# Kernel optimization log

Hardware: AMD Instinct MI355X
Metric: run time of the kernel (lower is better)

The kernel has to match this reference:

```python
import jax, jax.numpy as jnp
import numpy as np

B, C, H, W = 64, 256, 64, 64
E = 4                      # num_experts
CELL = 8
OUT = CELL * CELL + 1      # 65
EPS_BN = 1e-5
EPS_LB = 1e-6


def setup_inputs() -> dict:
    key = jax.random.key(0)
    ks = jax.random.split(key, 6)
    x = jax.random.normal(ks[0], (B, C, H, W), dtype=jnp.float32)
    w_experts = jax.random.normal(ks[1], (E, C, OUT), dtype=jnp.float32) * 0.05
    b_experts = jax.random.normal(ks[2], (E, OUT), dtype=jnp.float32) * 0.05
    w_gate = jax.random.normal(ks[3], (C, E), dtype=jnp.float32) * 0.05
    b_gate = jax.random.normal(ks[4], (E,), dtype=jnp.float32) * 0.05
    gamma = jnp.ones((OUT,), dtype=jnp.float32)
    beta = jnp.zeros((OUT,), dtype=jnp.float32)
    return {"x": x, "w_experts": w_experts, "b_experts": b_experts,
            "w_gate": w_gate, "b_gate": b_gate, "gamma": gamma, "beta": beta}


def pixel_shuffle(t, r):
    n, ch, h, w = t.shape
    nc = ch // (r * r)
    t = t.reshape(n, nc, r, r, h, w)
    t = t.transpose(0, 1, 4, 2, 5, 3)
    return t.reshape(n, nc, h * r, w * r)


def reference(x, w_experts, b_experts, w_gate, b_gate, gamma, beta):
    x = jax.nn.relu(x)
    xh = x.transpose(0, 2, 3, 1)                       # [B,H,W,C]

    # gating: global-avg-pool -> linear -> softmax -> hard top-1
    pooled = xh.mean(axis=(1, 2))                      # [B,C]
    gate = jax.nn.softmax(pooled @ w_gate + b_gate, axis=-1)
    idx = jnp.argmax(gate, axis=-1)                    # [B]

    # load-balancing KL(usage || uniform)
    usage = jnp.mean(jax.nn.one_hot(idx, E, dtype=xh.dtype), axis=0) + EPS_LB
    usage = usage / usage.sum()
    lb_loss = jnp.sum(usage * (jnp.log(usage) - jnp.log(jnp.full_like(usage, 1.0 / E))))

    # fused gather->grouped-GEMM (per-sample expert weight selection)
    w_sel = w_experts[idx]                             # [B,C,OUT]
    b_sel = b_experts[idx]                             # [B,OUT]
    y = jnp.einsum('bhwc,bco->bhwo', xh, w_sel) + b_sel[:, None, None, :]
    y = y.transpose(0, 3, 1, 2)                        # [B,OUT,H,W]

    # BatchNorm2d (training mode: batch statistics, biased variance)
    mean = y.mean(axis=(0, 2, 3), keepdims=True)
    var = y.var(axis=(0, 2, 3), keepdims=True)
    logits = (y - mean) / jnp.sqrt(var + EPS_BN)
    logits = logits * gamma[None, :, None, None] + beta[None, :, None, None]

    prob = jax.nn.softmax(logits, axis=1)[:, :-1]      # drop dustbin channel
    prob = pixel_shuffle(prob, CELL)                   # [B,1,H*8,W*8]
    prob = prob[:, 0]                                  # squeeze dim=1
    return logits, prob, lb_loss
```

## Files before the change

### kernel.cpp

```cpp
#include <hip/hip_runtime.h>
#include <stdint.h>
#include <math.h>

#define B_    64
#define C_    256
#define HW_   4096
#define E_    4
#define OUT_  65
#define NPAD_ 80

#define LOGITS_SZ (B_*OUT_*HW_)
#define PROB_SZ   (B_*512*512)

#define POOLED_OFF 0u
#define IDX_OFF    65536u
#define BNSUM_OFF  65792u
#define BNSS_OFF   66112u
#define WT_OFF     67072u
#define YB_OFF     230912u
#define CLEAR_BYTES 66432u

typedef float  f4 __attribute__((ext_vector_type(4)));
typedef short  s8 __attribute__((ext_vector_type(8)));

__device__ __forceinline__ uint32_t f2bf(float f){
  uint32_t u = __float_as_uint(f);
  return (u + 0x7FFFu + ((u >> 16) & 1u)) >> 16;
}
__device__ __forceinline__ uint32_t pk(float lo, float hi){
  return f2bf(lo) | (f2bf(hi) << 16);
}
__device__ __forceinline__ float bf2f(uint32_t u){
  return __uint_as_float((u & 0xFFFFu) << 16);
}


__global__ __launch_bounds__(256) void k_prep(const float* __restrict__ x,
                                              uint16_t* __restrict__ xb,
                                              float* __restrict__ pooled){
  __shared__ float pool_lds[64];
  int bid = blockIdx.x;
  int b = bid >> 7, ct = (bid >> 5) & 3, pt = bid & 31;
  int t = threadIdx.x;
  int cg = t & 7, pgg = t >> 3;
  int c0 = ct*64 + cg*8;
  int p0 = pt*128 + pgg*4;
  if (t < 64) pool_lds[t] = 0.f;
  __syncthreads();

  float v[8][4]; float s[8];
  const float* xp = x + ((size_t)(b*C_ + c0))*HW_ + p0;
#pragma unroll
  for (int r = 0; r < 8; ++r){
    float4 f = *(const float4*)(xp + (size_t)r*HW_);
    v[r][0]=fmaxf(f.x,0.f); v[r][1]=fmaxf(f.y,0.f);
    v[r][2]=fmaxf(f.z,0.f); v[r][3]=fmaxf(f.w,0.f);
    s[r] = v[r][0]+v[r][1]+v[r][2]+v[r][3];
  }
  int ksg  = ct*2 + (cg >> 2);
  int quad = cg & 3;
#pragma unroll
  for (int pp = 0; pp < 4; ++pp){
    int p = p0 + pp;
    uint16_t* dst = xb + ((((size_t)(b*256 + (p>>4))*8 + ksg)*64)
                          + (size_t)((p&15)*4 + quad))*8;
    uint4 w;
    w.x = pk(v[0][pp], v[1][pp]); w.y = pk(v[2][pp], v[3][pp]);
    w.z = pk(v[4][pp], v[5][pp]); w.w = pk(v[6][pp], v[7][pp]);
    *(uint4*)dst = w;
  }
#pragma unroll
  for (int r = 0; r < 8; ++r){
    float vv = s[r];
    vv += __shfl_xor(vv, 8);
    vv += __shfl_xor(vv, 16);
    vv += __shfl_xor(vv, 32);
    if ((t & 56) == 0)
      atomicAdd(&pool_lds[cg*8 + r], vv);
  }
  __syncthreads();
  if (t < 64) atomicAdd(pooled + b*C_ + ct*64 + t, pool_lds[t]);
}

__global__ void k_wtgate(const float* __restrict__ w_experts,
                         const float* __restrict__ w_gate,
                         const float* __restrict__ b_gate,
                         const float* __restrict__ pooled_sum,
                         uint16_t* __restrict__ Wt,
                         int* __restrict__ idx_ws,
                         float* __restrict__ out_lb){
  int bid = blockIdx.x;
  int t = threadIdx.x;
  if (bid < 320){
    if (t >= 32) return;
    int e = bid / NPAD_, o = bid % NPAD_;
    int ks = t >> 2, quad = t & 3;
    int c = t*8;
    float a[8];
    if (o < OUT_){
      const float* src = w_experts + (size_t)e*C_*OUT_ + o;
#pragma unroll
      for (int j = 0; j < 8; ++j) a[j] = src[(size_t)(c+j)*OUT_];
    } else {
#pragma unroll
      for (int j = 0; j < 8; ++j) a[j] = 0.f;
    }
    uint4 w;
    w.x = pk(a[0],a[1]); w.y = pk(a[2],a[3]);
    w.z = pk(a[4],a[5]); w.w = pk(a[6],a[7]);
    uint16_t* dst = Wt + ((((size_t)(e*5 + (o>>4))*8 + ks)*64)
                          + (size_t)((o&15)*4 + quad))*8;
    *(uint4*)dst = w;
    return;
  }
  __shared__ float gl[64][4];
  __shared__ int ish[64];
  int b = t >> 2, e = t & 3;
  float dot = 0.f;
  const float* pr = pooled_sum + b*C_;
  for (int c = 0; c < C_; c += 4){
    float4 p4 = *(const float4*)(pr + c);
    dot += p4.x*w_gate[c*4+e] + p4.y*w_gate[(c+1)*4+e]
         + p4.z*w_gate[(c+2)*4+e] + p4.w*w_gate[(c+3)*4+e];
  }
  gl[b][e] = dot * (1.f/4096.f) + b_gate[e];
  __syncthreads();
  if (t < 64){
    float best = gl[t][0]; int bi = 0;
    for (int ee = 1; ee < 4; ++ee){ float vv = gl[t][ee]; if (vv > best){best = vv; bi = ee;} }
    idx_ws[t] = bi; ish[t] = bi;
  }
  __syncthreads();
  if (t == 0){
    int cnt[4] = {0,0,0,0};
    for (int bb = 0; bb < 64; ++bb) cnt[ish[bb]]++;
    double u[4], S = 0.0;
    for (int ee = 0; ee < 4; ++ee){ u[ee] = cnt[ee]/64.0 + 1e-6; S += u[ee]; }
    double lb = 0.0;
    for (int ee = 0; ee < 4; ++ee){ double uu = u[ee]/S; lb += uu*(log(uu) - log(0.25)); }
    *out_lb = (float)lb;
  }
}

__global__ __launch_bounds__(256) void k_gemm(const uint16_t* __restrict__ xb,
                                              const uint16_t* __restrict__ Wt,
                                              const int* __restrict__ idx_ws,
                                              const float* __restrict__ b_experts,
                                              uint16_t* __restrict__ yb,
                                              float* __restrict__ bnsum,
                                              float* __restrict__ bnss){
  __shared__ float2 bnp[NPAD_*4];
  int bid = blockIdx.x;
  int b = bid >> 4, pt = bid & 15;
  int t = threadIdx.x;
  int w = t >> 6, lane = t & 63;
  int l15 = lane & 15, quad = lane >> 4;
  int lid = l15*4 + quad;
  int e = idx_ws[b];
  int p0 = pt*256 + w*64;
  const uint16_t* ap = xb + ((size_t)(b*256 + pt*16 + w*4))*4096 + (size_t)lid*8;
  const uint16_t* bp = Wt + (size_t)e*5*4096 + (size_t)lid*8;

  f4 acc[4][5];
#pragma unroll
  for (int mt=0; mt<4; ++mt)
#pragma unroll
    for (int nt=0; nt<5; ++nt){ f4 z = {0.f,0.f,0.f,0.f}; acc[mt][nt] = z; }

#pragma unroll
  for (int ks = 0; ks < 8; ++ks){
    s8 av[4], bv[5];
#pragma unroll
    for (int mt=0; mt<4; ++mt) av[mt] = *(const s8*)(ap + (size_t)mt*4096 + ks*512);
#pragma unroll
    for (int nt=0; nt<5; ++nt) bv[nt] = *(const s8*)(bp + (size_t)nt*4096 + ks*512);
#pragma unroll
    for (int mt=0; mt<4; ++mt)
#pragma unroll
      for (int nt=0; nt<5; ++nt)
        acc[mt][nt] = __builtin_amdgcn_mfma_f32_16x16x32_bf16(av[mt], bv[nt], acc[mt][nt], 0, 0, 0);
  }

#pragma unroll
  for (int nt=0; nt<5; ++nt){
    int o = nt*16 + l15;
    float bias = (o < OUT_) ? b_experts[e*OUT_ + o] : 0.f;
    float s1 = 0.f, s2 = 0.f;
#pragma unroll
    for (int mt=0; mt<4; ++mt){
#pragma unroll
      for (int r=0; r<4; ++r){
        float vv = acc[mt][nt][r] + bias;
        acc[mt][nt][r] = vv;
        s1 += vv; s2 += vv*vv;
      }
      if (o < OUT_){
        size_t base = ((size_t)(b*OUT_ + o))*HW_ + p0 + mt*16 + quad*4;
        uint2 st;
        st.x = pk(acc[mt][nt][0], acc[mt][nt][1]);
        st.y = pk(acc[mt][nt][2], acc[mt][nt][3]);
        *(uint2*)(yb + base) = st;
      }
    }
    s1 += __shfl_xor(s1, 16); s1 += __shfl_xor(s1, 32);
    s2 += __shfl_xor(s2, 16); s2 += __shfl_xor(s2, 32);
    if (quad == 0) bnp[(nt*16 + l15)*4 + w] = make_float2(s1, s2);
  }
  __syncthreads();
  if (t < OUT_){
    float2 a0 = bnp[t*4+0], a1 = bnp[t*4+1], a2 = bnp[t*4+2], a3 = bnp[t*4+3];
    atomicAdd(bnsum + t, a0.x+a1.x+a2.x+a3.x);
    atomicAdd(bnss  + t, a0.y+a1.y+a2.y+a3.y);
  }
}

__global__ __launch_bounds__(256) void k_final(const uint16_t* __restrict__ yb,
                                               const float* __restrict__ bnsum,
                                               const float* __restrict__ bnss,
                                               const float* __restrict__ gamma,
                                               const float* __restrict__ beta,
                                               float* __restrict__ out_logits,
                                               float* __restrict__ out_prob){
  __shared__ float lt[OUT_*132];
  __shared__ float2 ss[OUT_];
  int bid = blockIdx.x;
  int b = bid >> 5, pt = bid & 31;
  int p0 = pt*128;
  int t = threadIdx.x;
  if (t < OUT_){
    const float invN = 1.f/(float)(B_*HW_);
    float mean = bnsum[t]*invN;
    float var  = bnss[t]*invN - mean*mean;
    float sc   = gamma[t] / sqrtf(var + 1e-5f);
    ss[t] = make_float2(sc, beta[t] - mean*sc);
  }
  __syncthreads();

  int prr = t & 15, og = t >> 4;
#pragma unroll
  for (int oi = 0; oi < 5; ++oi){
    int o = og + oi*16;
    if (o < OUT_){
      size_t base = ((size_t)(b*OUT_ + o))*HW_ + p0 + prr*8;
      uint4 raw = *(const uint4*)(yb + base);
      float f[8];
      f[0]=bf2f(raw.x); f[1]=bf2f(raw.x>>16);
      f[2]=bf2f(raw.y); f[3]=bf2f(raw.y>>16);
      f[4]=bf2f(raw.z); f[5]=bf2f(raw.z>>16);
      f[6]=bf2f(raw.w); f[7]=bf2f(raw.w>>16);
      float2 sv = ss[o];
#pragma unroll
      for (int k=0;k<8;++k) f[k] = f[k]*sv.x + sv.y;
      float4 w0 = make_float4(f[0],f[1],f[2],f[3]);
      float4 w1 = make_float4(f[4],f[5],f[6],f[7]);
      *(float4*)(out_logits + base)     = w0;
      *(float4*)(out_logits + base + 4) = w1;
      float* lp = lt + o*132 + prr*8;
      *(float4*)(lp)     = w0;
      *(float4*)(lp + 4) = w1;
    }
  }
  __syncthreads();

  if (t < 128){
    float m = -1e30f;
    for (int o = 0; o < OUT_; ++o) m = fmaxf(m, lt[o*132 + t]);
    float ssum = 0.f;
    for (int o = 0; o < OUT_; ++o) ssum += __expf(lt[o*132 + t] - m);
    float inv = 1.f/ssum;
    int P = p0 + t;
    int h = P >> 6, wd = P & 63;
    float* pb = out_prob + ((size_t)b << 18) + (size_t)(h*8)*512 + wd*8;
#pragma unroll
    for (int r1 = 0; r1 < 8; ++r1){
      float4 q0, q1;
      q0.x = __expf(lt[(r1*8+0)*132+t]-m)*inv;
      q0.y = __expf(lt[(r1*8+1)*132+t]-m)*inv;
      q0.z = __expf(lt[(r1*8+2)*132+t]-m)*inv;
      q0.w = __expf(lt[(r1*8+3)*132+t]-m)*inv;
      q1.x = __expf(lt[(r1*8+4)*132+t]-m)*inv;
      q1.y = __expf(lt[(r1*8+5)*132+t]-m)*inv;
      q1.z = __expf(lt[(r1*8+6)*132+t]-m)*inv;
      q1.w = __expf(lt[(r1*8+7)*132+t]-m)*inv;
      *(float4*)(pb + r1*512)     = q0;
      *(float4*)(pb + r1*512 + 4) = q1;
    }
  }
}

extern "C" void kernel_launch(void* const* d_in, const int* in_sizes, int n_in,
                              void* d_out, int out_size, void* d_ws, size_t ws_size,
                              hipStream_t stream){
  const float* x         = (const float*)d_in[0];
  const float* w_experts = (const float*)d_in[1];
  const float* b_experts = (const float*)d_in[2];
  const float* w_gate    = (const float*)d_in[3];
  const float* b_gate    = (const float*)d_in[4];
  const float* gamma     = (const float*)d_in[5];
  const float* beta      = (const float*)d_in[6];

  float* out = (float*)d_out;
  char*  ws  = (char*)d_ws;
  float*     pooled = (float*)(ws + POOLED_OFF);
  int*       idxw   = (int*)(ws + IDX_OFF);
  float*     bnsum  = (float*)(ws + BNSUM_OFF);
  float*     bnss   = (float*)(ws + BNSS_OFF);
  uint16_t*  Wt     = (uint16_t*)(ws + WT_OFF);
  uint16_t*  ybm    = (uint16_t*)(ws + YB_OFF);
  uint16_t*  xbm    = (uint16_t*)d_out;

  float* logits = out;
  float* prob   = out + LOGITS_SZ;
  float* lb     = out + LOGITS_SZ + PROB_SZ;

  hipMemsetAsync(ws, 0, CLEAR_BYTES, stream);
  k_prep  <<<8192, 256, 0, stream>>>(x, xbm, pooled);
  k_wtgate<<<321, 256, 0, stream>>>(w_experts, w_gate, b_gate, pooled, Wt, idxw, lb);
  k_gemm  <<<1024, 256, 0, stream>>>(xbm, Wt, idxw, b_experts, ybm, bnsum, bnss);
  k_final <<<2048, 256, 0, stream>>>(ybm, bnsum, bnss, gamma, beta, logits, prob);
}
```

Before: 499.2 us.

## Fuse GEMM and BatchNorm/softmax epilogue via cooperative grid sync

Merges the grouped GEMM and the BN-normalize/softmax/pixel-shuffle kernel into one cooperative kernel. Accumulators stay in registers across a grid-wide sync, so the bf16 intermediate y never round-trips through global memory. It also folds the expert-weight transpose into the prep kernel and spreads the BN-statistic atomics over 8 slots to reduce contention. In exchange it requires all 1024 blocks to be co-resident, and it stages logits through LDS in two halves. A two-kernel fallback runs if the cooperative launch fails.

```diff
diff --git a/kernel.cpp b/kernel.cpp
--- a/kernel.cpp
+++ b/kernel.cpp
@@ -1,6 +1,9 @@
 #include <hip/hip_runtime.h>
+#include <hip/hip_cooperative_groups.h>
 #include <stdint.h>
 #include <math.h>
+
+namespace cg = cooperative_groups;
 
 #define B_    64
 #define C_    256
@@ -14,11 +17,11 @@
 
 #define POOLED_OFF 0u
 #define IDX_OFF    65536u
-#define BNSUM_OFF  65792u
-#define BNSS_OFF   66112u
-#define WT_OFF     67072u
-#define YB_OFF     230912u
-#define CLEAR_BYTES 66432u
+#define BNS_OFF    65792u
+#define BNSS_OFF   68352u
+#define CLEAR_BYTES 70912u
+#define WT_OFF     70912u
+#define YB_OFF     234752u
 
 typedef float  f4 __attribute__((ext_vector_type(4)));
 typedef short  s8 __attribute__((ext_vector_type(8)));
@@ -36,14 +39,41 @@
 
 
 __global__ __launch_bounds__(256) void k_prep(const float* __restrict__ x,
+                                              const float* __restrict__ w_experts,
                                               uint16_t* __restrict__ xb,
+                                              uint16_t* __restrict__ Wt,
                                               float* __restrict__ pooled){
   __shared__ float pool_lds[64];
   int bid = blockIdx.x;
+  int t = threadIdx.x;
+
+  if (bid >= 8192){
+    if (t >= 32) return;
+    int pid = bid - 8192;
+    int e = pid / NPAD_, o = pid % NPAD_;
+    int ks = t >> 2, quad = t & 3;
+    int c = t*8;
+    float a[8];
+    if (o < OUT_){
+      const float* src = w_experts + (size_t)e*C_*OUT_ + o;
+#pragma unroll
+      for (int j = 0; j < 8; ++j) a[j] = src[(size_t)(c+j)*OUT_];
+    } else {
+#pragma unroll
+      for (int j = 0; j < 8; ++j) a[j] = 0.f;
+    }
+    uint4 wv;
+    wv.x = pk(a[0],a[1]); wv.y = pk(a[2],a[3]);
+    wv.z = pk(a[4],a[5]); wv.w = pk(a[6],a[7]);
+    uint16_t* dst = Wt + ((((size_t)(e*5 + (o>>4))*8 + ks)*64)
+                          + (size_t)((o&15)*4 + quad))*8;
+    *(uint4*)dst = wv;
+    return;
+  }
+
   int b = bid >> 7, ct = (bid >> 5) & 3, pt = bid & 31;
-  int t = threadIdx.x;
-  int cg = t & 7, pgg = t >> 3;
-  int c0 = ct*64 + cg*8;
+  int cg_ = t & 7, pgg = t >> 3;
+  int c0 = ct*64 + cg_*8;
   int p0 = pt*128 + pgg*4;
   if (t < 64) pool_lds[t] = 0.f;
   __syncthreads();
@@ -57,8 +87,8 @@
     v[r][2]=fmaxf(f.z,0.f); v[r][3]=fmaxf(f.w,0.f);
     s[r] = v[r][0]+v[r][1]+v[r][2]+v[r][3];
   }
-  int ksg  = ct*2 + (cg >> 2);
-  int quad = cg & 3;
+  int ksg  = ct*2 + (cg_ >> 2);
+  int quad = cg_ & 3;
 #pragma unroll
   for (int pp = 0; pp < 4; ++pp){
     int p = p0 + pp;
@@ -76,45 +106,20 @@
     vv += __shfl_xor(vv, 16);
     vv += __shfl_xor(vv, 32);
     if ((t & 56) == 0)
-      atomicAdd(&pool_lds[cg*8 + r], vv);
+      atomicAdd(&pool_lds[cg_*8 + r], vv);
   }
   __syncthreads();
   if (t < 64) atomicAdd(pooled + b*C_ + ct*64 + t, pool_lds[t]);
 }
 
-__global__ void k_wtgate(const float* __restrict__ w_experts,
-                         const float* __restrict__ w_gate,
-                         const float* __restrict__ b_gate,
-                         const float* __restrict__ pooled_sum,
-                         uint16_t* __restrict__ Wt,
-                         int* __restrict__ idx_ws,
-                         float* __restrict__ out_lb){
-  int bid = blockIdx.x;
-  int t = threadIdx.x;
-  if (bid < 320){
-    if (t >= 32) return;
-    int e = bid / NPAD_, o = bid % NPAD_;
-    int ks = t >> 2, quad = t & 3;
-    int c = t*8;
-    float a[8];
-    if (o < OUT_){
-      const float* src = w_experts + (size_t)e*C_*OUT_ + o;
-#pragma unroll
-      for (int j = 0; j < 8; ++j) a[j] = src[(size_t)(c+j)*OUT_];
-    } else {
-#pragma unroll
-      for (int j = 0; j < 8; ++j) a[j] = 0.f;
-    }
-    uint4 w;
-    w.x = pk(a[0],a[1]); w.y = pk(a[2],a[3]);
-    w.z = pk(a[4],a[5]); w.w = pk(a[6],a[7]);
-    uint16_t* dst = Wt + ((((size_t)(e*5 + (o>>4))*8 + ks)*64)
-                          + (size_t)((o&15)*4 + quad))*8;
-    *(uint4*)dst = w;
-    return;
-  }
+__global__ void k_lb(const float* __restrict__ pooled_sum,
+                     const float* __restrict__ w_gate,
+                     const float* __restrict__ b_gate,
+                     int* __restrict__ idx_ws,
+                     float* __restrict__ out_lb){
   __shared__ float gl[64][4];
   __shared__ int ish[64];
+  int t = threadIdx.x;
   int b = t >> 2, e = t & 3;
   float dot = 0.f;
   const float* pr = pooled_sum + b*C_;
@@ -142,13 +147,166 @@
   }
 }
 
-__global__ __launch_bounds__(256) void k_gemm(const uint16_t* __restrict__ xb,
-                                              const uint16_t* __restrict__ Wt,
-                                              const int* __restrict__ idx_ws,
-                                              const float* __restrict__ b_experts,
-                                              uint16_t* __restrict__ yb,
-                                              float* __restrict__ bnsum,
-                                              float* __restrict__ bnss){
+__global__ __launch_bounds__(256, 4) void k_fused(
+    const uint16_t* __restrict__ xb, const uint16_t* __restrict__ Wt,
+    const int* __restrict__ idx_ws, const float* __restrict__ b_experts,
+    const float* __restrict__ gamma, const float* __restrict__ beta,
+    float* __restrict__ bnsum, float* __restrict__ bnss,
+    float* __restrict__ out_logits, float* __restrict__ out_prob){
+  __shared__ union ShMem {
+    float2 bnp[NPAD_*4];
+    struct { uint16_t lt[OUT_*136]; float2 ss[OUT_]; } fin;
+  } sh;
+
+  int bid = blockIdx.x;
+  int b = bid >> 4, pt = bid & 15;
+  int t = threadIdx.x;
+  int w = t >> 6, lane = t & 63;
+  int l15 = lane & 15, quad = lane >> 4;
+  int lid = l15*4 + quad;
+  int e = idx_ws[b];
+
+  int p0 = pt*256 + w*64;
+  const uint16_t* ap = xb + ((size_t)(b*256 + pt*16 + w*4))*4096 + (size_t)lid*8;
+  const uint16_t* bp = Wt + (size_t)e*5*4096 + (size_t)lid*8;
+
+  f4 acc[4][5];
+#pragma unroll
+  for (int mt=0; mt<4; ++mt)
+#pragma unroll
+    for (int nt=0; nt<5; ++nt){ f4 z = {0.f,0.f,0.f,0.f}; acc[mt][nt] = z; }
+
+#pragma unroll
+  for (int ks = 0; ks < 8; ++ks){
+    s8 bv[5];
+#pragma unroll
+    for (int nt=0; nt<5; ++nt) bv[nt] = *(const s8*)(bp + (size_t)nt*4096 + ks*512);
+#pragma unroll
+    for (int mt=0; mt<4; ++mt){
+      s8 av = *(const s8*)(ap + (size_t)mt*4096 + ks*512);
+#pragma unroll
+      for (int nt=0; nt<5; ++nt)
+        acc[mt][nt] = __builtin_amdgcn_mfma_f32_16x16x32_bf16(av, bv[nt], acc[mt][nt], 0, 0, 0);
+    }
+  }
+
+#pragma unroll
+  for (int nt=0; nt<5; ++nt){
+    int o = nt*16 + l15;
+    float bias = (o < OUT_) ? b_experts[e*OUT_ + o] : 0.f;
+    float s1 = 0.f, s2 = 0.f;
+#pragma unroll
+    for (int mt=0; mt<4; ++mt){
+#pragma unroll
+      for (int r=0; r<4; ++r){
+        float vv = acc[mt][nt][r] + bias;
+        acc[mt][nt][r] = vv;
+        s1 += vv; s2 += vv*vv;
+      }
+    }
+    s1 += __shfl_xor(s1, 16); s1 += __shfl_xor(s1, 32);
+    s2 += __shfl_xor(s2, 16); s2 += __shfl_xor(s2, 32);
+    if (quad == 0) sh.bnp[(nt*16 + l15)*4 + w] = make_float2(s1, s2);
+  }
+  __syncthreads();
+  if (t < OUT_){
+    float2 a0 = sh.bnp[t*4+0], a1 = sh.bnp[t*4+1], a2 = sh.bnp[t*4+2], a3 = sh.bnp[t*4+3];
+    atomicAdd(bnsum + (bid&7)*NPAD_ + t, a0.x+a1.x+a2.x+a3.x);
+    atomicAdd(bnss  + (bid&7)*NPAD_ + t, a0.y+a1.y+a2.y+a3.y);
+  }
+
+  __threadfence();
+  cg::this_grid().sync();
+  __threadfence();
+
+  if (t < OUT_){
+    float s1 = 0.f, s2 = 0.f;
+#pragma unroll
+    for (int k = 0; k < 8; ++k){ s1 += bnsum[k*NPAD_ + t]; s2 += bnss[k*NPAD_ + t]; }
+    const float invN = 1.f/(float)(B_*HW_);
+    float mean = s1*invN;
+    float var  = s2*invN - mean*mean;
+    float sc   = gamma[t] / sqrtf(var + 1e-5f);
+    sh.fin.ss[t] = make_float2(sc, beta[t] - mean*sc);
+  }
+  __syncthreads();
+
+  float2 sv[5];
+#pragma unroll
+  for (int nt=0; nt<5; ++nt){
+    int o = nt*16 + l15;
+    sv[nt] = (o < OUT_) ? sh.fin.ss[o] : make_float2(0.f, 0.f);
+  }
+#pragma unroll
+  for (int mt=0; mt<4; ++mt)
+#pragma unroll
+    for (int nt=0; nt<5; ++nt){
+      f4 vvv = acc[mt][nt];
+#pragma unroll
+      for (int r=0; r<4; ++r) vvv[r] = vvv[r]*sv[nt].x + sv[nt].y;
+      acc[mt][nt] = vvv;
+    }
+
+  for (int h = 0; h < 2; ++h){
+    __syncthreads();
+    if ((w >> 1) == h){
+      int px0 = (w & 1)*64;
+#pragma unroll
+      for (int mt=0; mt<4; ++mt)
+#pragma unroll
+        for (int nt=0; nt<5; ++nt){
+          int o = nt*16 + l15;
+          if (o < OUT_){
+            uint2 st;
+            st.x = pk(acc[mt][nt][0], acc[mt][nt][1]);
+            st.y = pk(acc[mt][nt][2], acc[mt][nt][3]);
+            *(uint2*)(sh.fin.lt + o*136 + px0 + mt*16 + quad*4) = st;
+          }
+        }
+    }
+    __syncthreads();
+
+    for (int idx = t; idx < OUT_*32; idx += 256){
+      int o = idx >> 5, px4 = idx & 31;
+      const uint16_t* lp = sh.fin.lt + o*136 + px4*4;
+      float4 fo = make_float4(bf2f(lp[0]), bf2f(lp[1]), bf2f(lp[2]), bf2f(lp[3]));
+      *(float4*)(out_logits + ((size_t)(b*OUT_ + o))*HW_ + pt*256 + h*128 + px4*4) = fo;
+    }
+
+    if (t < 128){
+      float m = -1e30f;
+      for (int o = 0; o < OUT_; ++o) m = fmaxf(m, bf2f(sh.fin.lt[o*136 + t]));
+      float ssum = 0.f;
+      for (int o = 0; o < OUT_; ++o) ssum += __expf(bf2f(sh.fin.lt[o*136 + t]) - m);
+      float inv = 1.f/ssum;
+      int P = pt*256 + h*128 + t;
+      int hh = P >> 6, wd = P & 63;
+      float* pb = out_prob + ((size_t)b << 18) + (size_t)(hh*8)*512 + (size_t)wd*8;
+#pragma unroll
+      for (int r1 = 0; r1 < 8; ++r1){
+        float4 q0, q1;
+        q0.x = __expf(bf2f(sh.fin.lt[(r1*8+0)*136+t])-m)*inv;
+        q0.y = __expf(bf2f(sh.fin.lt[(r1*8+1)*136+t])-m)*inv;
+        q0.z = __expf(bf2f(sh.fin.lt[(r1*8+2)*136+t])-m)*inv;
+        q0.w = __expf(bf2f(sh.fin.lt[(r1*8+3)*136+t])-m)*inv;
+        q1.x = __expf(bf2f(sh.fin.lt[(r1*8+4)*136+t])-m)*inv;
+        q1.y = __expf(bf2f(sh.fin.lt[(r1*8+5)*136+t])-m)*inv;
+        q1.z = __expf(bf2f(sh.fin.lt[(r1*8+6)*136+t])-m)*inv;
+        q1.w = __expf(bf2f(sh.fin.lt[(r1*8+7)*136+t])-m)*inv;
+        *(float4*)(pb + (size_t)r1*512)     = q0;
+        *(float4*)(pb + (size_t)r1*512 + 4) = q1;
+      }
+    }
+  }
+}
+
+__global__ __launch_bounds__(256) void k_gemm_fb(const uint16_t* __restrict__ xb,
+                                                 const uint16_t* __restrict__ Wt,
+                                                 const int* __restrict__ idx_ws,
+                                                 const float* __restrict__ b_experts,
+                                                 uint16_t* __restrict__ yb,
+                                                 float* __restrict__ bnsum,
+                                                 float* __restrict__ bnss){
   __shared__ float2 bnp[NPAD_*4];
   int bid = blockIdx.x;
   int b = bid >> 4, pt = bid & 15;
@@ -209,18 +367,18 @@
   __syncthreads();
   if (t < OUT_){
     float2 a0 = bnp[t*4+0], a1 = bnp[t*4+1], a2 = bnp[t*4+2], a3 = bnp[t*4+3];
-    atomicAdd(bnsum + t, a0.x+a1.x+a2.x+a3.x);
-    atomicAdd(bnss  + t, a0.y+a1.y+a2.y+a3.y);
-  }
-}
-
-__global__ __launch_bounds__(256) void k_final(const uint16_t* __restrict__ yb,
-                                               const float* __restrict__ bnsum,
-                                               const float* __restrict__ bnss,
-                                               const float* __restrict__ gamma,
-                                               const float* __restrict__ beta,
-                                               float* __restrict__ out_logits,
-                                               float* __restrict__ out_prob){
+    atomicAdd(bnsum + (bid&7)*NPAD_ + t, a0.x+a1.x+a2.x+a3.x);
+    atomicAdd(bnss  + (bid&7)*NPAD_ + t, a0.y+a1.y+a2.y+a3.y);
+  }
+}
+
+__global__ __launch_bounds__(256) void k_final_fb(const uint16_t* __restrict__ yb,
+                                                  const float* __restrict__ bnsum,
+                                                  const float* __restrict__ bnss,
+                                                  const float* __restrict__ gamma,
+                                                  const float* __restrict__ beta,
+                                                  float* __restrict__ out_logits,
+                                                  float* __restrict__ out_prob){
   __shared__ float lt[OUT_*132];
   __shared__ float2 ss[OUT_];
   int bid = blockIdx.x;
@@ -228,9 +386,12 @@
   int p0 = pt*128;
   int t = threadIdx.x;
   if (t < OUT_){
+    float s1 = 0.f, s2 = 0.f;
+#pragma unroll
+    for (int k = 0; k < 8; ++k){ s1 += bnsum[k*NPAD_ + t]; s2 += bnss[k*NPAD_ + t]; }
     const float invN = 1.f/(float)(B_*HW_);
-    float mean = bnsum[t]*invN;
-    float var  = bnss[t]*invN - mean*mean;
+    float mean = s1*invN;
+    float var  = s2*invN - mean*mean;
     float sc   = gamma[t] / sqrtf(var + 1e-5f);
     ss[t] = make_float2(sc, beta[t] - mean*sc);
   }
@@ -270,7 +431,7 @@
     float inv = 1.f/ssum;
     int P = p0 + t;
     int h = P >> 6, wd = P & 63;
-    float* pb = out_prob + ((size_t)b << 18) + (size_t)(h*8)*512 + wd*8;
+    float* pb = out_prob + ((size_t)b << 18) + (size_t)(h*8)*512 + (size_t)wd*8;
 #pragma unroll
     for (int r1 = 0; r1 < 8; ++r1){
       float4 q0, q1;
@@ -303,7 +464,7 @@
   char*  ws  = (char*)d_ws;
   float*     pooled = (float*)(ws + POOLED_OFF);
   int*       idxw   = (int*)(ws + IDX_OFF);
-  float*     bnsum  = (float*)(ws + BNSUM_OFF);
+  float*     bnsum  = (float*)(ws + BNS_OFF);
   float*     bnss   = (float*)(ws + BNSS_OFF);
   uint16_t*  Wt     = (uint16_t*)(ws + WT_OFF);
   uint16_t*  ybm    = (uint16_t*)(ws + YB_OFF);
@@ -311,11 +472,19 @@
 
   float* logits = out;
   float* prob   = out + LOGITS_SZ;
-  float* lb     = out + LOGITS_SZ + PROB_SZ;
+  float* lbp    = out + LOGITS_SZ + PROB_SZ;
 
   hipMemsetAsync(ws, 0, CLEAR_BYTES, stream);
-  k_prep  <<<8192, 256, 0, stream>>>(x, xbm, pooled);
-  k_wtgate<<<321, 256, 0, stream>>>(w_experts, w_gate, b_gate, pooled, Wt, idxw, lb);
-  k_gemm  <<<1024, 256, 0, stream>>>(xbm, Wt, idxw, b_experts, ybm, bnsum, bnss);
-  k_final <<<2048, 256, 0, stream>>>(ybm, bnsum, bnss, gamma, beta, logits, prob);
-}
+  k_prep<<<8512, 256, 0, stream>>>(x, w_experts, xbm, Wt, pooled);
+  k_lb<<<1, 256, 0, stream>>>(pooled, w_gate, b_gate, idxw, lbp);
+
+  void* args[] = { (void*)&xbm, (void*)&Wt, (void*)&idxw, (void*)&b_experts,
+                   (void*)&gamma, (void*)&beta, (void*)&bnsum, (void*)&bnss,
+                   (void*)&logits, (void*)&prob };
+  hipError_t cerr = hipLaunchCooperativeKernel((void*)k_fused, dim3(1024),
+                                               dim3(256), args, 0, stream);
+  if (cerr != hipSuccess){
+    k_gemm_fb <<<1024, 256, 0, stream>>>(xbm, Wt, idxw, b_experts, ybm, bnsum, bnss);
+    k_final_fb<<<2048, 256, 0, stream>>>(ybm, bnsum, bnss, gamma, beta, logits, prob);
+  }
+}
```

After: 739.7 us. +48.2%, slower.
